# Kernel optimization log

Hardware: AMD Instinct MI355X
Metric: run time of the kernel (lower is better)

Reference implementation:

```python
import math
import jax, jax.numpy as jnp
import numpy as np

B, C, T = 4, 512, 1024
H = 8
KC = C // H
WIN = 4


def _get_relative_embeddings(emb, length):
    win = (emb.shape[1] - 1) // 2
    pad_length = max(length - (win + 1), 0)
    slice_start = max(win + 1 - length, 0)
    slice_end = slice_start + 2 * length - 1
    if pad_length > 0:
        emb = jnp.pad(emb, ((0, 0), (pad_length, pad_length), (0, 0)))
    return emb[:, slice_start:slice_end]


def _relative_to_absolute(x):
    # x: [b, h, L, 2L-1] -> [b, h, L, L] via skew trick
    b, h, L, _ = x.shape
    x = jnp.pad(x, ((0, 0), (0, 0), (0, 0), (0, 1)))          # [b,h,L,2L]
    x_flat = x.reshape(b, h, L * 2 * L)
    x_flat = jnp.pad(x_flat, ((0, 0), (0, 0), (0, L - 1)))    # [b,h,(L+1)(2L-1)]
    x_final = x_flat.reshape(b, h, L + 1, 2 * L - 1)
    return x_final[:, :, :L, L - 1:]


def _absolute_to_relative(x):
    # x: [b, h, L, L] -> [b, h, L, 2L-1]
    b, h, L, _ = x.shape
    x = jnp.pad(x, ((0, 0), (0, 0), (0, 0), (0, L - 1)))      # [b,h,L,2L-1]
    x_flat = x.reshape(b, h, L * (2 * L - 1))
    x_flat = jnp.pad(x_flat, ((0, 0), (0, 0), (L, 0)))        # [b,h,2L^2]
    x_final = x_flat.reshape(b, h, L, 2 * L)
    return x_final[:, :, :, 1:]


def setup_inputs() -> dict:
    key = jax.random.key(0)
    ks = jax.random.split(key, 12)
    xavier = math.sqrt(6.0 / (C + C))  # xavier_uniform for [C, C, 1] conv weight
    rel_std = KC ** (-0.5)
    return {
        "x": jax.random.normal(ks[0], (B, C, T), dtype=jnp.float32),
        "wq": jax.random.uniform(ks[1], (C, C), jnp.float32, -xavier, xavier),
        "bq": jnp.zeros((C,), jnp.float32),
        "wk": jax.random.uniform(ks[2], (C, C), jnp.float32, -xavier, xavier),
        "bk": jnp.zeros((C,), jnp.float32),
        "wv": jax.random.uniform(ks[3], (C, C), jnp.float32, -xavier, xavier),
        "bv": jnp.zeros((C,), jnp.float32),
        "wo": jax.random.normal(ks[4], (C, C), jnp.float32) * (1.0 / math.sqrt(C)),
        "bo": jnp.zeros((C,), jnp.float32),
        "emb_rel_k": jax.random.normal(ks[5], (1, 2 * WIN + 1, KC), jnp.float32) * rel_std,
        "emb_rel_v": jax.random.normal(ks[6], (1, 2 * WIN + 1, KC), jnp.float32) * rel_std,
    }


def reference(x, wq, bq, wk, bk, wv, bv, wo, bo, emb_rel_k, emb_rel_v):
    b, c, t = x.shape
    # 1x1 conv == channel matmul
    q = jnp.einsum("oi,bit->bot", wq, x) + bq[:, None]
    k = jnp.einsum("oi,bit->bot", wk, x) + bk[:, None]
    v = jnp.einsum("oi,bit->bot", wv, x) + bv[:, None]
    # [b, H, t, kc]
    q = q.reshape(b, H, KC, t).transpose(0, 1, 3, 2)
    k = k.reshape(b, H, KC, t).transpose(0, 1, 3, 2)
    v = v.reshape(b, H, KC, t).transpose(0, 1, 3, 2)
    inv_sqrt = 1.0 / math.sqrt(KC)
    scores = jnp.einsum("bhtc,bhsc->bhts", q, k) * inv_sqrt
    rel_k = _get_relative_embeddings(emb_rel_k, t)[0]            # [2t-1, kc]
    rel_logits = jnp.einsum("bhtc,rc->bhtr", q, rel_k)           # [b,h,t,2t-1]
    scores = scores + _relative_to_absolute(rel_logits) * inv_sqrt
    p_attn = jax.nn.softmax(scores, axis=-1)
    output = jnp.einsum("bhts,bhsc->bhtc", p_attn, v)
    rel_weights = _absolute_to_relative(p_attn)                  # [b,h,t,2t-1]
    rel_v = _get_relative_embeddings(emb_rel_v, t)[0]            # [2t-1, kc]
    output = output + jnp.einsum("bhtr,rc->bhtc", rel_weights, rel_v)
    output = output.transpose(0, 1, 3, 2).reshape(b, c, t)
    return jnp.einsum("oi,bit->bot", wo, output) + bo[:, None]
```

## Files before the change

kernel.cpp:

```cpp
#include <hip/hip_runtime.h>
#include <hip/hip_bf16.h>

#define Bdim 4
#define Cdim 512
#define Tdim 1024
#define Hn   8
#define KCd  64

#define QK_SCALE 0.18033688011112042f

typedef __attribute__((ext_vector_type(8))) short bf16x8;
typedef __attribute__((ext_vector_type(4))) float f32x4;

__device__ __forceinline__ unsigned short f32_bf16_rne(float f) {
    unsigned u = __float_as_uint(f);
    u += 0x7FFFu + ((u >> 16) & 1u);
    return (unsigned short)(u >> 16);
}
__device__ __forceinline__ float bf16_f32(unsigned short h) {
    return __uint_as_float(((unsigned)h) << 16);
}
__device__ __forceinline__ void split8(const float* f, bf16x8& h8, bf16x8& l8) {
    #pragma unroll
    for (int e = 0; e < 8; ++e) {
        const unsigned short hh = f32_bf16_rne(f[e]);
        h8[e] = (short)hh;
        l8[e] = (short)f32_bf16_rne(f[e] - bf16_f32(hh));
    }
}

__device__ __forceinline__ int sw(int row, int col) {
    return (row << 6) + ((((col >> 3) ^ (row & 7)) << 3) | (col & 7));
}
__device__ __forceinline__ bf16x8 fragld(const unsigned short* a, int row, int kstep, int quad) {
    return *(const bf16x8*)&a[(row << 6) + ((((kstep << 2) | quad) ^ (row & 7)) << 3)];
}


__global__ __launch_bounds__(256) void prep_kernel(
    const float* __restrict__ wq, const float* __restrict__ wk,
    const float* __restrict__ wv, const float* __restrict__ wo,
    const float* __restrict__ x,
    unsigned short* __restrict__ WAhi, unsigned short* __restrict__ WAlo,
    unsigned short* __restrict__ XBhi, unsigned short* __restrict__ XBlo)
{
    const int w = threadIdx.x >> 6, lane = threadIdx.x & 63;
    const int l15 = lane & 15, quad = lane >> 4;
    const int task = blockIdx.x * 4 + w;

    if (task < 2048) {
        const int mtile = task >> 4, kt = task & 15;
        const int sel = mtile >> 5;
        const float* W = sel == 0 ? wq : (sel == 1 ? wk : (sel == 2 ? wv : wo));
        const int row = (mtile & 31) * 16 + l15;
        const float* p = W + (size_t)row * Cdim + kt * 32 + quad * 8;
        float f[8];
        *(float4*)&f[0] = *(const float4*)p;
        *(float4*)&f[4] = *(const float4*)(p + 4);
        bf16x8 h8, l8;
        split8(f, h8, l8);
        const size_t base = (size_t)task * 512 + lane * 8;
        *(bf16x8*)(WAhi + base) = h8;
        *(bf16x8*)(WAlo + base) = l8;
    } else {
        const int t2 = task - 2048;
        const int b = t2 >> 10, ntile = (t2 >> 4) & 63, kt = t2 & 15;
        const float* Xb = x + (size_t)b * Cdim * Tdim;
        const int n = ntile * 16 + l15;
        const int k0 = kt * 32 + quad * 8;
        float f[8];
        #pragma unroll
        for (int e = 0; e < 8; ++e) f[e] = Xb[(size_t)(k0 + e) * Tdim + n];
        bf16x8 h8, l8;
        split8(f, h8, l8);
        const size_t base = (size_t)t2 * 512 + lane * 8;
        *(bf16x8*)(XBhi + base) = h8;
        *(bf16x8*)(XBlo + base) = l8;
    }
}

__global__ __launch_bounds__(256, 3) void gemm_qkv(
    const unsigned short* __restrict__ Ahi, const unsigned short* __restrict__ Alo,
    const unsigned short* __restrict__ Bhi, const unsigned short* __restrict__ Blo,
    const float* __restrict__ bq, const float* __restrict__ bk, const float* __restrict__ bv,
    unsigned short* __restrict__ qhi, unsigned short* __restrict__ qlo,
    unsigned short* __restrict__ khi, unsigned short* __restrict__ klo,
    unsigned short* __restrict__ vhi, unsigned short* __restrict__ vlo)
{
    __shared__ alignas(16) unsigned short As[2][4][2][512];

    const int tid = threadIdx.x;
    const int w = tid >> 6, lane = tid & 63;
    const int l15 = lane & 15, quad = lane >> 4;
    const int lo8 = lane << 3;

    const int id = blockIdx.x;
    const int xcd = id & 7, slot = id >> 3;
    const int m64 = slot >> 2;
    const int col128 = xcd * 4 + (slot & 3);
    const int col = col128 * 4 + w;
    const int b = col >> 5, n32 = col & 31;
    const int sel = m64 >> 3;
    const int mtb = m64 * 4;
    const int ntb = b * 64 + n32 * 2;

    const unsigned short* Asrc_h = Ahi + (size_t)(mtb + w) * 8192 + lo8;
    const unsigned short* Asrc_l = Alo + (size_t)(mtb + w) * 8192 + lo8;

    f32x4 acc[4][2];
    #pragma unroll
    for (int i = 0; i < 4; ++i)
        #pragma unroll
        for (int j = 0; j < 2; ++j) acc[i][j] = (f32x4){0.f, 0.f, 0.f, 0.f};

    bf16x8 Bh[2][2], Bl[2][2];
    #pragma unroll
    for (int nt = 0; nt < 2; ++nt) {
        const size_t o = (size_t)(ntb + nt) * 8192 + lo8;
        Bh[0][nt] = *(const bf16x8*)(Bhi + o);
        Bl[0][nt] = *(const bf16x8*)(Blo + o);
    }
    *(bf16x8*)&As[0][w][0][lo8] = *(const bf16x8*)Asrc_h;
    *(bf16x8*)&As[0][w][1][lo8] = *(const bf16x8*)Asrc_l;
    __syncthreads();

    for (int kt = 0; kt < 16; ++kt) {
        const int cur = kt & 1, nxt = cur ^ 1;
        bf16x8 stgh, stgl;
        if (kt < 15) {
            const int kn = (kt + 1) * 512;
            stgh = *(const bf16x8*)(Asrc_h + kn);
            stgl = *(const bf16x8*)(Asrc_l + kn);
            #pragma unroll
            for (int nt = 0; nt < 2; ++nt) {
                const size_t o = (size_t)(ntb + nt) * 8192 + kn + lo8;
                Bh[nxt][nt] = *(const bf16x8*)(Bhi + o);
                Bl[nxt][nt] = *(const bf16x8*)(Blo + o);
            }
        }
        bf16x8 Afh[4], Afl[4];
        #pragma unroll
        for (int mt = 0; mt < 4; ++mt) {
            Afh[mt] = *(const bf16x8*)&As[cur][mt][0][lo8];
            Afl[mt] = *(const bf16x8*)&As[cur][mt][1][lo8];
        }
        #pragma unroll
        for (int mt = 0; mt < 4; ++mt)
            #pragma unroll
            for (int nt = 0; nt < 2; ++nt) {
                f32x4 c = acc[mt][nt];
                c = __builtin_amdgcn_mfma_f32_16x16x32_bf16(Afh[mt], Bh[cur][nt], c, 0, 0, 0);
                c = __builtin_amdgcn_mfma_f32_16x16x32_bf16(Afh[mt], Bl[cur][nt], c, 0, 0, 0);
                c = __builtin_amdgcn_mfma_f32_16x16x32_bf16(Afl[mt], Bh[cur][nt], c, 0, 0, 0);
                acc[mt][nt] = c;
            }
        if (kt < 15) {
            *(bf16x8*)&As[nxt][w][0][lo8] = stgh;
            *(bf16x8*)&As[nxt][w][1][lo8] = stgl;
        }
        __syncthreads();
    }

    const int head = m64 & 7;
    const size_t hbase = ((size_t)(b * Hn + head) * 16) << 12;
    if (sel < 2) {
        const float* Bv = sel == 0 ? bq : bk;
        unsigned short* ph = sel == 0 ? qhi : khi;
        unsigned short* pl = sel == 0 ? qlo : klo;
        const float qscale = sel == 0 ? QK_SCALE : 1.0f;
        #pragma unroll
        for (int mt = 0; mt < 4; ++mt) {
            const int c0 = mt * 16 + quad * 4;
            float bb[4];
            #pragma unroll
            for (int r = 0; r < 4; ++r) bb[r] = Bv[head * 64 + c0 + r];
            const int lane_out = (((c0 >> 3) & 3) << 4) + l15;
            const int e0 = c0 & 7;
            const int cg = c0 >> 5;
            #pragma unroll
            for (int nt = 0; nt < 2; ++nt) {
                const int tile = n32 >> 1;
                const int rhi = (n32 & 1) * 2 + nt;
                const int g = rhi * 2 + cg;
                const size_t off = hbase + ((size_t)tile << 12) + g * 512
                                 + (size_t)lane_out * 8 + e0;
                ushort4 h4, l4;
                #pragma unroll
                for (int r = 0; r < 4; ++r) {
                    const float v = (acc[mt][nt][r] + bb[r]) * qscale;
                    const unsigned short hh = f32_bf16_rne(v);
                    ((unsigned short*)&h4)[r] = hh;
                    ((unsigned short*)&l4)[r] = f32_bf16_rne(v - bf16_f32(hh));
                }
                *(ushort4*)(ph + off) = h4;
                *(ushort4*)(pl + off) = l4;
            }
        }
    } else {
        #pragma unroll
        for (int mt = 0; mt < 4; ++mt) {
            const int c0 = mt * 16 + quad * 4;
            float bb[4];
            #pragma unroll
            for (int r = 0; r < 4; ++r) bb[r] = bv[head * 64 + c0 + r];
            #pragma unroll
            for (int nt = 0; nt < 2; ++nt) {
                const int t = n32 * 32 + nt * 16 + l15;
                const int tile = t >> 6, jl = t & 63;
                const int jg = jl >> 5, lanej = ((jl >> 3) & 3) << 4;
                const int e = jl & 7;
                const size_t tb = hbase + ((size_t)tile << 12);
                #pragma unroll
                for (int r = 0; r < 4; ++r) {
                    const int c = c0 + r;
                    const int g = mt * 2 + jg;
                    const int lane_v = lanej + (c & 15);
                    const float v = acc[mt][nt][r] + bb[r];
                    const unsigned short hh = f32_bf16_rne(v);
                    const size_t off = tb + g * 512 + (size_t)lane_v * 8 + e;
                    vhi[off] = hh;
                    vlo[off] = f32_bf16_rne(v - bf16_f32(hh));
                }
            }
        }
    }
}

__global__ __launch_bounds__(256) void gemm_out(
    const unsigned short* __restrict__ Ahi, const unsigned short* __restrict__ Alo,
    const unsigned short* __restrict__ Bhi, const unsigned short* __restrict__ Blo,
    const float* __restrict__ bo, float* __restrict__ out)
{
    __shared__ alignas(16) unsigned short Bs[2][2][2][512];

    const int tid = threadIdx.x;
    const int w = tid >> 6, lane = tid & 63;
    const int l15 = lane & 15, quad = lane >> 4;
    const int lo8 = lane << 3;

    const int id = blockIdx.x;
    const int xcd = id & 7, slot = id >> 3;
    const int col = xcd * 16 + (slot >> 2);
    const int mg  = slot & 3;
    const int b = col >> 5, n32 = col & 31;
    const int m32 = mg * 4 + w;
    const int mtb = 96 + m32 * 2;
    const int ntb = b * 64 + n32 * 2;

    const unsigned short* Bsrc =
        ((w & 1) ? Blo : Bhi) + (size_t)(ntb + (w >> 1)) * 8192 + lo8;

    f32x4 acc[2][2];
    #pragma unroll
    for (int i = 0; i < 2; ++i)
        #pragma unroll
        for (int j = 0; j < 2; ++j) acc[i][j] = (f32x4){0.f, 0.f, 0.f, 0.f};

    bf16x8 Ah[2][2], Al[2][2];
    #pragma unroll
    for (int mt = 0; mt < 2; ++mt) {
        const size_t o = (size_t)(mtb + mt) * 8192 + lo8;
        Ah[0][mt] = *(const bf16x8*)(Ahi + o);
        Al[0][mt] = *(const bf16x8*)(Alo + o);
    }
    *(bf16x8*)&Bs[0][w >> 1][w & 1][lo8] = *(const bf16x8*)Bsrc;
    __syncthreads();

    for (int kt = 0; kt < 16; ++kt) {
        const int cur = kt & 1, nxt = cur ^ 1;
        bf16x8 stg;
        if (kt < 15) {
            const int kn = (kt + 1) * 512;
            stg = *(const bf16x8*)(Bsrc + kn);
            #pragma unroll
            for (int mt = 0; mt < 2; ++mt) {
                const size_t o = (size_t)(mtb + mt) * 8192 + kn + lo8;
                Ah[nxt][mt] = *(const bf16x8*)(Ahi + o);
                Al[nxt][mt] = *(const bf16x8*)(Alo + o);
            }
        }
        bf16x8 Bfh[2], Bfl[2];
        #pragma unroll
        for (int nt = 0; nt < 2; ++nt) {
            Bfh[nt] = *(const bf16x8*)&Bs[cur][nt][0][lo8];
            Bfl[nt] = *(const bf16x8*)&Bs[cur][nt][1][lo8];
        }
        #pragma unroll
        for (int mt = 0; mt < 2; ++mt)
            #pragma unroll
            for (int nt = 0; nt < 2; ++nt) {
                f32x4 c = acc[mt][nt];
                c = __builtin_amdgcn_mfma_f32_16x16x32_bf16(Ah[cur][mt], Bfh[nt], c, 0, 0, 0);
                c = __builtin_amdgcn_mfma_f32_16x16x32_bf16(Ah[cur][mt], Bfl[nt], c, 0, 0, 0);
                c = __builtin_amdgcn_mfma_f32_16x16x32_bf16(Al[cur][mt], Bfh[nt], c, 0, 0, 0);
                acc[mt][nt] = c;
            }
        if (kt < 15) {
            *(bf16x8*)&Bs[nxt][w >> 1][w & 1][lo8] = stg;
        }
        __syncthreads();
    }

    float* Ob = out + (size_t)b * Cdim * Tdim;
    #pragma unroll
    for (int mt = 0; mt < 2; ++mt) {
        const int m = m32 * 32 + mt * 16 + quad * 4;
        float bb[4];
        #pragma unroll
        for (int r = 0; r < 4; ++r) bb[r] = bo[m + r];
        #pragma unroll
        for (int nt = 0; nt < 2; ++nt) {
            const int t = n32 * 32 + nt * 16 + l15;
            #pragma unroll
            for (int r = 0; r < 4; ++r)
                Ob[(size_t)(m + r) * Tdim + t] = acc[mt][nt][r] + bb[r];
        }
    }
}

__global__ __launch_bounds__(256) void attn_mfma(
    const unsigned short* __restrict__ qhi, const unsigned short* __restrict__ qlo,
    const unsigned short* __restrict__ khi, const unsigned short* __restrict__ klo,
    const unsigned short* __restrict__ vhi, const unsigned short* __restrict__ vlo,
    const float* __restrict__ ek,
    const float* __restrict__ ev,
    unsigned short* __restrict__ cxhi, unsigned short* __restrict__ cxlo)
{
    __shared__ alignas(16) unsigned short psh[4096], psl[4096];
    __shared__ float rk[576];
    __shared__ float evs[576];
    __shared__ float bandp[576];

    const int tid = threadIdx.x;
    int it, h, b;
    {
        const int n = blockIdx.x;
        const int xcd = n & 7, slot = n >> 3;
        const int pair = (xcd << 2) | (slot >> 4);
        it = slot & 15;
        b = pair >> 3;
        h = pair & 7;
    }
    const int i0 = it * 64;
    const int lane = tid & 63, w = tid >> 6;
    const int l15 = lane & 15, quad = lane >> 4;
    const int m_blk = w * 16 + l15;
    const int lo8 = lane << 3;

    const size_t bh16 = (size_t)(b * Hn + h) * 16;

    bf16x8 qfh[2], qfl[2];
    {
        const unsigned short* qth = qhi + ((bh16 + it) << 12);
        const unsigned short* qtl = qlo + ((bh16 + it) << 12);
        #pragma unroll
        for (int ks = 0; ks < 2; ++ks) {
            qfh[ks] = *(const bf16x8*)(qth + (((w << 1) | ks) << 9) + lo8);
            qfl[ks] = *(const bf16x8*)(qtl + (((w << 1) | ks) << 9) + lo8);
        }
    }

    bf16x8 ekh[2], ekl[2];
    #pragma unroll
    for (int ks = 0; ks < 2; ++ks) {
        #pragma unroll
        for (int j = 0; j < 8; ++j) { ekh[ks][j] = 0; ekl[ks][j] = 0; }
        if (l15 < 9) {
            #pragma unroll
            for (int j = 0; j < 8; ++j) {
                const float v = ek[l15 * 64 + ks * 32 + quad * 8 + j];
                const unsigned short hh = f32_bf16_rne(v);
                ekh[ks][j] = (short)hh;
                ekl[ks][j] = (short)f32_bf16_rne(v - bf16_f32(hh));
            }
        }
    }

    {
        f32x4 rkD = (f32x4){0.f, 0.f, 0.f, 0.f};
        #pragma unroll
        for (int ks = 0; ks < 2; ++ks) {
            rkD = __builtin_amdgcn_mfma_f32_16x16x32_bf16(qfh[ks], ekh[ks], rkD, 0, 0, 0);
            rkD = __builtin_amdgcn_mfma_f32_16x16x32_bf16(qfh[ks], ekl[ks], rkD, 0, 0, 0);
            rkD = __builtin_amdgcn_mfma_f32_16x16x32_bf16(qfl[ks], ekh[ks], rkD, 0, 0, 0);
        }
        if (l15 < 9) {
            #pragma unroll
            for (int r = 0; r < 4; ++r)
                rk[(w * 16 + quad * 4 + r) * 9 + l15] = rkD[r];
        }
    }
    for (int idx = tid; idx < 576; idx += 256) evs[idx] = ev[idx];
    __syncthreads();

    float m_run = -1e30f, l_run = 0.f;
    f32x4 Oc[4];
    #pragma unroll
    for (int ct = 0; ct < 4; ++ct) Oc[ct] = (f32x4){0.f, 0.f, 0.f, 0.f};

    const unsigned short* kh0 = khi + (bh16 << 12);
    const unsigned short* kl0 = klo + (bh16 << 12);
    const unsigned short* vh0 = vhi + (bh16 << 12);
    const unsigned short* vl0 = vlo + (bh16 << 12);

    for (int t = 0; t < 16; ++t) {
        const int j0 = t << 6;
        const size_t tb = (size_t)t << 12;
        const unsigned short* kht = kh0 + tb;
        const unsigned short* klt = kl0 + tb;
        const unsigned short* vht = vh0 + tb;
        const unsigned short* vlt = vl0 + tb;

        bf16x8 vbh[2][4], vbl[2][4];
        #pragma unroll
        for (int ks = 0; ks < 2; ++ks)
            #pragma unroll
            for (int ct = 0; ct < 4; ++ct) {
                vbh[ks][ct] = *(const bf16x8*)(vht + (((ct << 1) | ks) << 9) + lo8);
                vbl[ks][ct] = *(const bf16x8*)(vlt + (((ct << 1) | ks) << 9) + lo8);
            }

        f32x4 Sc[4];
        #pragma unroll
        for (int jt = 0; jt < 4; ++jt) Sc[jt] = (f32x4){0.f, 0.f, 0.f, 0.f};
        #pragma unroll
        for (int ks = 0; ks < 2; ++ks) {
            bf16x8 ah[4], al[4];
            #pragma unroll
            for (int jt = 0; jt < 4; ++jt) {
                ah[jt] = *(const bf16x8*)(kht + (((jt << 1) | ks) << 9) + lo8);
                al[jt] = *(const bf16x8*)(klt + (((jt << 1) | ks) << 9) + lo8);
            }
            #pragma unroll
            for (int jt = 0; jt < 4; ++jt) {
                Sc[jt] = __builtin_amdgcn_mfma_f32_16x16x32_bf16(ah[jt], qfh[ks], Sc[jt], 0, 0, 0);
                Sc[jt] = __builtin_amdgcn_mfma_f32_16x16x32_bf16(ah[jt], qfl[ks], Sc[jt], 0, 0, 0);
                Sc[jt] = __builtin_amdgcn_mfma_f32_16x16x32_bf16(al[jt], qfh[ks], Sc[jt], 0, 0, 0);
            }
        }

        const int dt = j0 - i0;
        const bool diag = (dt >= -67 && dt <= 67);
        if (diag) {
            #pragma unroll
            for (int jt = 0; jt < 4; ++jt) {
                const int db = dt + jt * 16 + quad * 4 - m_blk;
                #pragma unroll
                for (int r = 0; r < 4; ++r) {
                    const int d = db + r;
                    if ((unsigned)(d + 4) <= 8u) Sc[jt][r] += rk[m_blk * 9 + d + 4];
                }
            }
        }

        const float mt = fmaxf(
            fmaxf(fmaxf(fmaxf(Sc[0][0], Sc[0][1]), fmaxf(Sc[0][2], Sc[0][3])),
                  fmaxf(fmaxf(Sc[1][0], Sc[1][1]), fmaxf(Sc[1][2], Sc[1][3]))),
            fmaxf(fmaxf(fmaxf(Sc[2][0], Sc[2][1]), fmaxf(Sc[2][2], Sc[2][3])),
                  fmaxf(fmaxf(Sc[3][0], Sc[3][1]), fmaxf(Sc[3][2], Sc[3][3]))));
        float mr = fmaxf(mt, __shfl_xor(mt, 16));
        mr = fmaxf(mr, __shfl_xor(mr, 32));
        const float mn = fmaxf(m_run, mr);
        const float alpha = __builtin_amdgcn_exp2f(m_run - mn);

        #pragma unroll
        for (int jt = 0; jt < 4; ++jt)
            #pragma unroll
            for (int r = 0; r < 4; ++r)
                Sc[jt][r] = __builtin_amdgcn_exp2f(Sc[jt][r] - mn);

        float rs = ((Sc[0][0] + Sc[0][1]) + (Sc[0][2] + Sc[0][3]))
                 + ((Sc[1][0] + Sc[1][1]) + (Sc[1][2] + Sc[1][3]))
                 + ((Sc[2][0] + Sc[2][1]) + (Sc[2][2] + Sc[2][3]))
                 + ((Sc[3][0] + Sc[3][1]) + (Sc[3][2] + Sc[3][3]));
        rs += __shfl_xor(rs, 16);
        rs += __shfl_xor(rs, 32);
        l_run = l_run * alpha + rs;
        m_run = mn;

        if (diag) {
            #pragma unroll
            for (int jt = 0; jt < 4; ++jt) {
                const int db = dt + jt * 16 + quad * 4 - m_blk;
                #pragma unroll
                for (int r = 0; r < 4; ++r) {
                    const int d = db + r;
                    if ((unsigned)(d + 4) <= 8u) bandp[m_blk * 9 + d + 4] = Sc[jt][r];
                }
            }
        }

        #pragma unroll
        for (int jt = 0; jt < 4; ++jt) {
            ushort4 ph, pl;
            ph.x = f32_bf16_rne(Sc[jt][0]); pl.x = f32_bf16_rne(Sc[jt][0] - bf16_f32(ph.x));
            ph.y = f32_bf16_rne(Sc[jt][1]); pl.y = f32_bf16_rne(Sc[jt][1] - bf16_f32(ph.y));
            ph.z = f32_bf16_rne(Sc[jt][2]); pl.z = f32_bf16_rne(Sc[jt][2] - bf16_f32(ph.z));
            ph.w = f32_bf16_rne(Sc[jt][3]); pl.w = f32_bf16_rne(Sc[jt][3] - bf16_f32(ph.w));
            const int o = sw(m_blk, jt * 16 + quad * 4);
            *(ushort4*)&psh[o] = ph;
            *(ushort4*)&psl[o] = pl;
        }

        const float al0 = __shfl(alpha, quad * 4 + 0);
        const float al1 = __shfl(alpha, quad * 4 + 1);
        const float al2 = __shfl(alpha, quad * 4 + 2);
        const float al3 = __shfl(alpha, quad * 4 + 3);
        #pragma unroll
        for (int ct = 0; ct < 4; ++ct) {
            Oc[ct][0] *= al0; Oc[ct][1] *= al1; Oc[ct][2] *= al2; Oc[ct][3] *= al3;
        }
        #pragma unroll
        for (int ks = 0; ks < 2; ++ks) {
            bf16x8 pah = fragld(psh, m_blk, ks, quad);
            bf16x8 pal = fragld(psl, m_blk, ks, quad);
            #pragma unroll
            for (int ct = 0; ct < 4; ++ct) {
                Oc[ct] = __builtin_amdgcn_mfma_f32_16x16x32_bf16(pah, vbh[ks][ct], Oc[ct], 0, 0, 0);
                Oc[ct] = __builtin_amdgcn_mfma_f32_16x16x32_bf16(pah, vbl[ks][ct], Oc[ct], 0, 0, 0);
                Oc[ct] = __builtin_amdgcn_mfma_f32_16x16x32_bf16(pal, vbh[ks][ct], Oc[ct], 0, 0, 0);
            }
        }

        if (diag) {
            #pragma unroll
            for (int r = 0; r < 4; ++r) {
                const int mrow = w * 16 + quad * 4 + r;
                const int ig = i0 + mrow;
                #pragma unroll
                for (int e = 0; e < 9; ++e) {
                    const int jl = ig + e - 4 - j0;
                    if ((unsigned)jl < 64u) {
                        const float p = bandp[mrow * 9 + e];
                        #pragma unroll
                        for (int ct = 0; ct < 4; ++ct)
                            Oc[ct][r] += p * evs[e * 64 + ct * 16 + l15];
                    }
                }
            }
        }
    }

    const float rlv = 1.f / l_run;
    float rl[4];
    rl[0] = __shfl(rlv, quad * 4 + 0);
    rl[1] = __shfl(rlv, quad * 4 + 1);
    rl[2] = __shfl(rlv, quad * 4 + 2);
    rl[3] = __shfl(rlv, quad * 4 + 3);
    const int ntile16 = it * 4 + w;
    const int e = l15 & 7;
    #pragma unroll
    for (int ct = 0; ct < 4; ++ct) {
        const int cl = ct * 16 + l15;
        const int ktc = h * 2 + (cl >> 5);
        const int lane_c = (((ct * 2 + (l15 >> 3)) & 3) << 4) + quad * 4;
        const size_t base = (((size_t)(b * 64 + ntile16)) * 16 + ktc) * 512;
        #pragma unroll
        for (int r = 0; r < 4; ++r) {
            const float v = Oc[ct][r] * rl[r];
            const unsigned short hh = f32_bf16_rne(v);
            const size_t off = base + (size_t)(lane_c + r) * 8 + e;
            cxhi[off] = hh;
            cxlo[off] = f32_bf16_rne(v - bf16_f32(hh));
        }
    }
}

extern "C" void kernel_launch(void* const* d_in, const int* in_sizes, int n_in,
                              void* d_out, int out_size, void* d_ws, size_t ws_size,
                              hipStream_t stream) {
    const float* x  = (const float*)d_in[0];
    const float* wq = (const float*)d_in[1];
    const float* bq = (const float*)d_in[2];
    const float* wk = (const float*)d_in[3];
    const float* bk = (const float*)d_in[4];
    const float* wv = (const float*)d_in[5];
    const float* bv = (const float*)d_in[6];
    const float* wo = (const float*)d_in[7];
    const float* bo = (const float*)d_in[8];
    const float* ek = (const float*)d_in[9];
    const float* ev = (const float*)d_in[10];
    float* out = (float*)d_out;

    const size_t PW = 2048u * 512u;
    const size_t PX = 4u * 1024u * 512u;
    unsigned short* WAhi = (unsigned short*)d_ws;
    unsigned short* WAlo = WAhi + PW;
    unsigned short* XBhi = WAlo + PW;
    unsigned short* XBlo = XBhi + PX;
    unsigned short* qhi  = XBlo + PX;
    unsigned short* qlo  = qhi + PX;
    unsigned short* khi  = qlo + PX;
    unsigned short* klo  = khi + PX;
    unsigned short* vhi  = klo + PX;
    unsigned short* vlo  = vhi + PX;
    unsigned short* cxhi = vlo + PX;
    unsigned short* cxlo = cxhi + PX;

    prep_kernel<<<dim3(1536), 256, 0, stream>>>(
        wq, wk, wv, wo, x, WAhi, WAlo, XBhi, XBlo);

    gemm_qkv<<<dim3(768), 256, 0, stream>>>(
        WAhi, WAlo, XBhi, XBlo, bq, bk, bv,
        qhi, qlo, khi, klo, vhi, vlo);

    attn_mfma<<<dim3(512), 256, 0, stream>>>(
        qhi, qlo, khi, klo, vhi, vlo, ek, ev, cxhi, cxlo);

    gemm_out<<<dim3(512), 256, 0, stream>>>(
        WAhi, WAlo, cxhi, cxlo, bo, out);
}
```

Measured before the change: 162.1 us.

## Split attention KV range across two blocks and merge partials in new kernel

```diff
diff --git a/kernel.cpp b/kernel.cpp
--- a/kernel.cpp
+++ b/kernel.cpp
@@ -324,7 +324,8 @@
     const unsigned short* __restrict__ vhi, const unsigned short* __restrict__ vlo,
     const float* __restrict__ ek,
     const float* __restrict__ ev,
-    unsigned short* __restrict__ cxhi, unsigned short* __restrict__ cxlo)
+    float* __restrict__ pO,
+    float* __restrict__ pML)
 {
     __shared__ alignas(16) unsigned short psh[4096], psl[4096];
     __shared__ float rk[576];
@@ -332,12 +333,13 @@
     __shared__ float bandp[576];
 
     const int tid = threadIdx.x;
-    int it, h, b;
+    int it, h, b, s;
     {
         const int n = blockIdx.x;
         const int xcd = n & 7, slot = n >> 3;
-        const int pair = (xcd << 2) | (slot >> 4);
-        it = slot & 15;
+        const int pair = (xcd << 2) | (slot >> 5);
+        it = (slot >> 1) & 15;
+        s  = slot & 1;
         b = pair >> 3;
         h = pair & 7;
     }
@@ -348,6 +350,7 @@
     const int lo8 = lane << 3;
 
     const size_t bh16 = (size_t)(b * Hn + h) * 16;
+    const int pidx = (((b * Hn + h) * 16 + it) << 1) | s;
 
     bf16x8 qfh[2], qfl[2];
     {
@@ -360,23 +363,23 @@
         }
     }
 
-    bf16x8 ekh[2], ekl[2];
-    #pragma unroll
-    for (int ks = 0; ks < 2; ++ks) {
-        #pragma unroll
-        for (int j = 0; j < 8; ++j) { ekh[ks][j] = 0; ekl[ks][j] = 0; }
-        if (l15 < 9) {
-            #pragma unroll
-            for (int j = 0; j < 8; ++j) {
-                const float v = ek[l15 * 64 + ks * 32 + quad * 8 + j];
-                const unsigned short hh = f32_bf16_rne(v);
-                ekh[ks][j] = (short)hh;
-                ekl[ks][j] = (short)f32_bf16_rne(v - bf16_f32(hh));
-            }
-        }
-    }
-
-    {
+    const bool anyDiag = (s == 0) ? (it <= 8) : (it >= 7);
+    if (anyDiag) {
+        bf16x8 ekh[2], ekl[2];
+        #pragma unroll
+        for (int ks = 0; ks < 2; ++ks) {
+            #pragma unroll
+            for (int j = 0; j < 8; ++j) { ekh[ks][j] = 0; ekl[ks][j] = 0; }
+            if (l15 < 9) {
+                #pragma unroll
+                for (int j = 0; j < 8; ++j) {
+                    const float v = ek[l15 * 64 + ks * 32 + quad * 8 + j];
+                    const unsigned short hh = f32_bf16_rne(v);
+                    ekh[ks][j] = (short)hh;
+                    ekl[ks][j] = (short)f32_bf16_rne(v - bf16_f32(hh));
+                }
+            }
+        }
         f32x4 rkD = (f32x4){0.f, 0.f, 0.f, 0.f};
         #pragma unroll
         for (int ks = 0; ks < 2; ++ks) {
@@ -389,9 +392,9 @@
             for (int r = 0; r < 4; ++r)
                 rk[(w * 16 + quad * 4 + r) * 9 + l15] = rkD[r];
         }
-    }
-    for (int idx = tid; idx < 576; idx += 256) evs[idx] = ev[idx];
-    __syncthreads();
+        for (int idx = tid; idx < 576; idx += 256) evs[idx] = ev[idx];
+        __syncthreads();
+    }
 
     float m_run = -1e30f, l_run = 0.f;
     f32x4 Oc[4];
@@ -403,7 +406,9 @@
     const unsigned short* vh0 = vhi + (bh16 << 12);
     const unsigned short* vl0 = vlo + (bh16 << 12);
 
-    for (int t = 0; t < 16; ++t) {
+    const int t0 = s << 3;
+    for (int tt = 0; tt < 8; ++tt) {
+        const int t = t0 + tt;
         const int j0 = t << 6;
         const size_t tb = (size_t)t << 12;
         const unsigned short* kht = kh0 + tb;
@@ -541,12 +546,47 @@
         }
     }
 
-    const float rlv = 1.f / l_run;
-    float rl[4];
-    rl[0] = __shfl(rlv, quad * 4 + 0);
-    rl[1] = __shfl(rlv, quad * 4 + 1);
-    rl[2] = __shfl(rlv, quad * 4 + 2);
-    rl[3] = __shfl(rlv, quad * 4 + 3);
+    float* pOp = pO + ((size_t)pidx << 12) + (w << 10) + lane;
+    #pragma unroll
+    for (int ct = 0; ct < 4; ++ct)
+        #pragma unroll
+        for (int r = 0; r < 4; ++r)
+            pOp[(ct * 4 + r) << 6] = Oc[ct][r];
+    float* pMLp = pML + ((size_t)pidx << 9) + (w << 7) + lane;
+    pMLp[0]  = m_run;
+    pMLp[64] = l_run;
+}
+
+__global__ __launch_bounds__(256) void attn_merge(
+    const float* __restrict__ pO, const float* __restrict__ pML,
+    unsigned short* __restrict__ cxhi, unsigned short* __restrict__ cxlo)
+{
+    const int tid = threadIdx.x;
+    const int w = tid >> 6, lane = tid & 63;
+    const int l15 = lane & 15, quad = lane >> 4;
+    const int idx = blockIdx.x;
+    const int it = idx & 15, h = (idx >> 4) & 7, b = idx >> 7;
+
+    const float* ml0 = pML + (((size_t)idx << 1) << 9) + (w << 7);
+    const float* ml1 = ml0 + 512;
+    const float m0 = ml0[lane], l0 = ml0[64 + lane];
+    const float m1 = ml1[lane], l1 = ml1[64 + lane];
+    const float mm = fmaxf(m0, m1);
+    const float a0 = __builtin_amdgcn_exp2f(m0 - mm);
+    const float a1 = __builtin_amdgcn_exp2f(m1 - mm);
+    const float rlv = 1.f / (l0 * a0 + l1 * a1);
+
+    float a0r[4], a1r[4], rl[4];
+    #pragma unroll
+    for (int r = 0; r < 4; ++r) {
+        a0r[r] = __shfl(a0, quad * 4 + r);
+        a1r[r] = __shfl(a1, quad * 4 + r);
+        rl[r]  = __shfl(rlv, quad * 4 + r);
+    }
+
+    const float* O0 = pO + (((size_t)idx << 1) << 12) + (w << 10) + lane;
+    const float* O1 = O0 + 4096;
+
     const int ntile16 = it * 4 + w;
     const int e = l15 & 7;
     #pragma unroll
@@ -557,7 +597,8 @@
         const size_t base = (((size_t)(b * 64 + ntile16)) * 16 + ktc) * 512;
         #pragma unroll
         for (int r = 0; r < 4; ++r) {
-            const float v = Oc[ct][r] * rl[r];
+            const float v = (O0[(ct * 4 + r) << 6] * a0r[r]
+                           + O1[(ct * 4 + r) << 6] * a1r[r]) * rl[r];
             const unsigned short hh = f32_bf16_rne(v);
             const size_t off = base + (size_t)(lane_c + r) * 8 + e;
             cxhi[off] = hh;
@@ -596,6 +637,8 @@
     unsigned short* vlo  = vhi + PX;
     unsigned short* cxhi = vlo + PX;
     unsigned short* cxlo = cxhi + PX;
+    float* pO  = (float*)(cxlo + PX);
+    float* pML = pO + 1024u * 4096u;
 
     prep_kernel<<<dim3(1536), 256, 0, stream>>>(
         wq, wk, wv, wo, x, WAhi, WAlo, XBhi, XBlo);
@@ -604,8 +647,10 @@
         WAhi, WAlo, XBhi, XBlo, bq, bk, bv,
         qhi, qlo, khi, klo, vhi, vlo);
 
-    attn_mfma<<<dim3(512), 256, 0, stream>>>(
-        qhi, qlo, khi, klo, vhi, vlo, ek, ev, cxhi, cxlo);
+    attn_mfma<<<dim3(1024), 256, 0, stream>>>(
+        qhi, qlo, khi, klo, vhi, vlo, ek, ev, pO, pML);
+
+    attn_merge<<<dim3(512), 256, 0, stream>>>(pO, pML, cxhi, cxlo);
 
     gemm_out<<<dim3(512), 256, 0, stream>>>(
         WAhi, WAlo, cxhi, cxlo, bo, out);
```

Result: slower. 173.8 us (+7.2%).

## Stage K/V tiles into LDS with global_load_lds shared across waves

Applied to the files above, without the earlier changes.

```diff
diff --git a/kernel.cpp b/kernel.cpp
--- a/kernel.cpp
+++ b/kernel.cpp
@@ -27,6 +27,13 @@
         h8[e] = (short)hh;
         l8[e] = (short)f32_bf16_rne(f[e] - bf16_f32(hh));
     }
+}
+
+__device__ __forceinline__ void gload16(const unsigned short* g, unsigned short* l) {
+    __builtin_amdgcn_global_load_lds(
+        (const __attribute__((address_space(1))) unsigned int*)g,
+        (__attribute__((address_space(3))) unsigned int*)l,
+        16, 0, 0);
 }
 
 __device__ __forceinline__ int sw(int row, int col) {
@@ -327,6 +334,8 @@
     unsigned short* __restrict__ cxhi, unsigned short* __restrict__ cxlo)
 {
     __shared__ alignas(16) unsigned short psh[4096], psl[4096];
+    __shared__ alignas(16) unsigned short KsH[4096], KsL[4096];
+    __shared__ alignas(16) unsigned short VsH[4096], VsL[4096];
     __shared__ float rk[576];
     __shared__ float evs[576];
     __shared__ float bandp[576];
@@ -349,6 +358,20 @@
 
     const size_t bh16 = (size_t)(b * Hn + h) * 16;
 
+    const unsigned short* kh0 = khi + (bh16 << 12);
+    const unsigned short* kl0 = klo + (bh16 << 12);
+    const unsigned short* vh0 = vhi + (bh16 << 12);
+    const unsigned short* vl0 = vlo + (bh16 << 12);
+
+    const unsigned short* splane =
+        (w == 0) ? kh0 : (w == 1) ? kl0 : (w == 2) ? vh0 : vl0;
+    unsigned short* dplane =
+        (w == 0) ? KsH : (w == 1) ? KsL : (w == 2) ? VsH : VsL;
+
+    #pragma unroll
+    for (int g = 0; g < 8; ++g)
+        gload16(splane + (g << 9) + lo8, dplane + (g << 9));
+
     bf16x8 qfh[2], qfl[2];
     {
         const unsigned short* qth = qhi + ((bh16 + it) << 12);
@@ -398,27 +421,8 @@
     #pragma unroll
     for (int ct = 0; ct < 4; ++ct) Oc[ct] = (f32x4){0.f, 0.f, 0.f, 0.f};
 
-    const unsigned short* kh0 = khi + (bh16 << 12);
-    const unsigned short* kl0 = klo + (bh16 << 12);
-    const unsigned short* vh0 = vhi + (bh16 << 12);
-    const unsigned short* vl0 = vlo + (bh16 << 12);
-
     for (int t = 0; t < 16; ++t) {
         const int j0 = t << 6;
-        const size_t tb = (size_t)t << 12;
-        const unsigned short* kht = kh0 + tb;
-        const unsigned short* klt = kl0 + tb;
-        const unsigned short* vht = vh0 + tb;
-        const unsigned short* vlt = vl0 + tb;
-
-        bf16x8 vbh[2][4], vbl[2][4];
-        #pragma unroll
-        for (int ks = 0; ks < 2; ++ks)
-            #pragma unroll
-            for (int ct = 0; ct < 4; ++ct) {
-                vbh[ks][ct] = *(const bf16x8*)(vht + (((ct << 1) | ks) << 9) + lo8);
-                vbl[ks][ct] = *(const bf16x8*)(vlt + (((ct << 1) | ks) << 9) + lo8);
-            }
 
         f32x4 Sc[4];
         #pragma unroll
@@ -428,8 +432,8 @@
             bf16x8 ah[4], al[4];
             #pragma unroll
             for (int jt = 0; jt < 4; ++jt) {
-                ah[jt] = *(const bf16x8*)(kht + (((jt << 1) | ks) << 9) + lo8);
-                al[jt] = *(const bf16x8*)(klt + (((jt << 1) | ks) << 9) + lo8);
+                ah[jt] = *(const bf16x8*)&KsH[(((jt << 1) | ks) << 9) + lo8];
+                al[jt] = *(const bf16x8*)&KsL[(((jt << 1) | ks) << 9) + lo8];
             }
             #pragma unroll
             for (int jt = 0; jt < 4; ++jt) {
@@ -516,9 +520,11 @@
             bf16x8 pal = fragld(psl, m_blk, ks, quad);
             #pragma unroll
             for (int ct = 0; ct < 4; ++ct) {
-                Oc[ct] = __builtin_amdgcn_mfma_f32_16x16x32_bf16(pah, vbh[ks][ct], Oc[ct], 0, 0, 0);
-                Oc[ct] = __builtin_amdgcn_mfma_f32_16x16x32_bf16(pah, vbl[ks][ct], Oc[ct], 0, 0, 0);
-                Oc[ct] = __builtin_amdgcn_mfma_f32_16x16x32_bf16(pal, vbh[ks][ct], Oc[ct], 0, 0, 0);
+                bf16x8 vh = *(const bf16x8*)&VsH[(((ct << 1) | ks) << 9) + lo8];
+                bf16x8 vl = *(const bf16x8*)&VsL[(((ct << 1) | ks) << 9) + lo8];
+                Oc[ct] = __builtin_amdgcn_mfma_f32_16x16x32_bf16(pah, vh, Oc[ct], 0, 0, 0);
+                Oc[ct] = __builtin_amdgcn_mfma_f32_16x16x32_bf16(pah, vl, Oc[ct], 0, 0, 0);
+                Oc[ct] = __builtin_amdgcn_mfma_f32_16x16x32_bf16(pal, vh, Oc[ct], 0, 0, 0);
             }
         }
 
@@ -538,6 +544,15 @@
                     }
                 }
             }
+        }
+
+        __syncthreads();
+        if (t < 15) {
+            const size_t tb = (size_t)(t + 1) << 12;
+            #pragma unroll
+            for (int g = 0; g < 8; ++g)
+                gload16(splane + tb + (g << 9) + lo8, dplane + (g << 9));
+            __syncthreads();
         }
     }
 
```

Result: no change. 164.6 us (+1.6%).
